# Optimization experiments

Measured on AMD Instinct MI355X. Metric: run time of the kernel, lower is better.

Reference implementation:

```python
import jax, jax.numpy as jnp
import numpy as np

FORWARD_BITS = 8
R_MAX = 0.01
SIGMA0_FWD = 2.0 ** (6 - FORWARD_BITS)  # 0.25, per DynamicFixedQuantizer.__init__


def _rescale(data, sigma, bit, r_max):
    """Dynamic range adjustment: doubles sigma on overflow, halves on underflow."""
    half = 2.0 ** (bit - 1)
    t_max = sigma * half - sigma
    t_min = -sigma * half
    n = jnp.float32(data.size)
    overflow = (jnp.sum(data > t_max) + jnp.sum(data < t_min)).astype(jnp.float32) / n
    underflow = (jnp.sum(data > 0.5 * t_max) + jnp.sum(data < 0.5 * t_min)).astype(jnp.float32) / n
    sigma = jnp.where(overflow > r_max, sigma * 2.0,
                      jnp.where(underflow < r_max, sigma * 0.5, sigma))
    t_max = sigma * half - sigma
    t_min = -sigma * half
    return sigma, t_min, t_max


def _stochastic_round(data, sigma, t_min, t_max, key):
    # temp = floor(data/sigma + U[0,1)) * sigma, then clamp -- fused elementwise chain
    r = jax.random.uniform(key, data.shape, dtype=data.dtype)
    temp = jnp.floor(data / sigma + r) * sigma
    return jnp.clip(temp, t_min, t_max)


def setup_inputs() -> dict:
    key = jax.random.key(0)
    x = jax.random.normal(key, (32, 2048, 2048), dtype=jnp.float32)
    return {"x": x}


def reference(x):
    sigma = jnp.float32(SIGMA0_FWD)
    sigma, t_min, t_max = _rescale(x, sigma, FORWARD_BITS, R_MAX)
    # forward always uses stochastic rounding in the original code
    rkey = jax.random.fold_in(jax.random.key(42), 0)
    return _stochastic_round(x, sigma, t_min, t_max, rkey)
```

## Files before the change

### kernel.cpp

```cpp
#include <hip/hip_runtime.h>
#include <stdint.h>

typedef float floatx4 __attribute__((ext_vector_type(4)));

static inline void threefry2x32_host(uint32_t k0, uint32_t k1,
                                     uint32_t x0, uint32_t x1,
                                     uint32_t& o0, uint32_t& o1) {
  const uint32_t ks2 = k0 ^ k1 ^ 0x1BD11BDAu;
#define TF_ROUND(r) { x0 += x1; x1 = (x1 << (r)) | (x1 >> (32 - (r))); x1 ^= x0; }
  x0 += k0; x1 += k1;
  TF_ROUND(13) TF_ROUND(15) TF_ROUND(26) TF_ROUND(6)
  x0 += k1;  x1 += ks2 + 1u;
  TF_ROUND(17) TF_ROUND(29) TF_ROUND(16) TF_ROUND(24)
  x0 += ks2; x1 += k0 + 2u;
  TF_ROUND(13) TF_ROUND(15) TF_ROUND(26) TF_ROUND(6)
  x0 += k0;  x1 += k1 + 3u;
  TF_ROUND(17) TF_ROUND(29) TF_ROUND(16) TF_ROUND(24)
  x0 += k1;  x1 += ks2 + 4u;
  TF_ROUND(13) TF_ROUND(15) TF_ROUND(26) TF_ROUND(6)
  x0 += ks2; x1 += k0 + 5u;
#undef TF_ROUND
  o0 = x0; o1 = x1;
}

__device__ __forceinline__ uint32_t tf_bits(uint32_t x1, uint32_t k0,
                                            uint32_t k1, uint32_t ks2) {
  uint32_t x0 = k0;
#define R4(a,b,c,d)                                              \
  x0 += x1; x1 = __builtin_rotateleft32(x1, a); x1 ^= x0;        \
  x0 += x1; x1 = __builtin_rotateleft32(x1, b); x1 ^= x0;        \
  x0 += x1; x1 = __builtin_rotateleft32(x1, c); x1 ^= x0;        \
  x0 += x1; x1 = __builtin_rotateleft32(x1, d); x1 ^= x0;
  R4(13, 15, 26, 6)
  x0 += k1;  x1 += ks2 + 1u;
  R4(17, 29, 16, 24)
  x0 += ks2; x1 += k0 + 2u;
  R4(13, 15, 26, 6)
  x0 += k0;  x1 += k1 + 3u;
  R4(17, 29, 16, 24)
  x0 += k1;  x1 += ks2 + 4u;
  R4(13, 15, 26, 6)
  x0 += ks2; x1 += k0 + 5u;
#undef R4
  return x0 ^ x1;
}

__device__ __forceinline__ float qround(float v, uint32_t bits, float sigma,
                                        float inv_sigma, float tmin, float tmax) {
  float r = __uint_as_float((bits >> 9) | 0x3f800000u) - 1.0f;
  float t = floorf(__builtin_fmaf(v, inv_sigma, r)) * sigma;
  return fminf(fmaxf(t, tmin), tmax);
}

__global__ __launch_bounds__(256) void count_kernel(
    const float4* __restrict__ x4, const float* __restrict__ x,
    long long n4, long long n, unsigned int* __restrict__ counts,
    float tmax, float tmin, float htmax, float htmin) {
  long long idx = (long long)blockIdx.x * 256 + threadIdx.x;
  long long stride = (long long)gridDim.x * 256;
  unsigned int over = 0, under = 0;
  for (long long i = idx; i < n4; i += stride) {
    float4 v = x4[i];
    over  += __popcll(__ballot(v.x > tmax))  + __popcll(__ballot(v.x < tmin))
           + __popcll(__ballot(v.y > tmax))  + __popcll(__ballot(v.y < tmin))
           + __popcll(__ballot(v.z > tmax))  + __popcll(__ballot(v.z < tmin))
           + __popcll(__ballot(v.w > tmax))  + __popcll(__ballot(v.w < tmin));
    under += __popcll(__ballot(v.x > htmax)) + __popcll(__ballot(v.x < htmin))
           + __popcll(__ballot(v.y > htmax)) + __popcll(__ballot(v.y < htmin))
           + __popcll(__ballot(v.z > htmax)) + __popcll(__ballot(v.z < htmin))
           + __popcll(__ballot(v.w > htmax)) + __popcll(__ballot(v.w < htmin));
  }
  if ((threadIdx.x & 63) == 0) {
    if (over)  atomicAdd(&counts[0], over);
    if (under) atomicAdd(&counts[1], under);
  }
  if (idx == 0 && (n & 3)) {
    unsigned int o2 = 0, u2 = 0;
    for (long long j = n4 << 2; j < n; ++j) {
      float v = x[j];
      o2 += (v > tmax)  + (v < tmin);
      u2 += (v > htmax) + (v < htmin);
    }
    if (o2) atomicAdd(&counts[0], o2);
    if (u2) atomicAdd(&counts[1], u2);
  }
}

__global__ __launch_bounds__(256) void quant_kernel(
    const float4* __restrict__ x4, floatx4* __restrict__ o4,
    const float* __restrict__ x, float* __restrict__ out,
    long long n4, long long n, const unsigned int* __restrict__ counts,
    float inv_n, uint32_t k0, uint32_t k1) {
  const uint32_t ks2 = k0 ^ k1 ^ 0x1BD11BDAu;
  float overflow  = (float)counts[0] * inv_n;
  float underflow = (float)counts[1] * inv_n;
  float sigma = (overflow > 0.01f) ? 0.5f
              : ((underflow < 0.01f) ? 0.125f : 0.25f);
  float tmax = sigma * 128.0f - sigma;
  float tmin = sigma * -128.0f;
  float inv_sigma = 1.0f / sigma;

  long long idx = (long long)blockIdx.x * 256 + threadIdx.x;
  long long stride = (long long)gridDim.x * 256;
  if (idx < n4) {
    long long i = idx + ((n4 - 1 - idx) / stride) * stride;
    for (; i >= idx; i -= stride) {
      float4 v = x4[i];
      uint32_t s = ((uint32_t)i << 2) + k1;
      uint32_t b0 = tf_bits(s + 0u, k0, k1, ks2);
      uint32_t b1 = tf_bits(s + 1u, k0, k1, ks2);
      uint32_t b2 = tf_bits(s + 2u, k0, k1, ks2);
      uint32_t b3 = tf_bits(s + 3u, k0, k1, ks2);
      floatx4 r;
      r.x = qround(v.x, b0, sigma, inv_sigma, tmin, tmax);
      r.y = qround(v.y, b1, sigma, inv_sigma, tmin, tmax);
      r.z = qround(v.z, b2, sigma, inv_sigma, tmin, tmax);
      r.w = qround(v.w, b3, sigma, inv_sigma, tmin, tmax);
      __builtin_nontemporal_store(r, &o4[i]);
    }
  }
  if (idx == 0 && (n & 3)) {
    for (long long j = n4 << 2; j < n; ++j) {
      uint32_t b = tf_bits((uint32_t)j + k1, k0, k1, ks2);
      out[j] = qround(x[j], b, sigma, inv_sigma, tmin, tmax);
    }
  }
}

extern "C" void kernel_launch(void* const* d_in, const int* in_sizes, int n_in,
                              void* d_out, int out_size, void* d_ws, size_t ws_size,
                              hipStream_t stream) {
  const float* x = (const float*)d_in[0];
  float* out = (float*)d_out;
  long long n = (long long)in_sizes[0];

  unsigned int* counts = (unsigned int*)d_ws;
  (void)hipMemsetAsync(counts, 0, 2 * sizeof(unsigned int), stream);

  uint32_t k0, k1;
  threefry2x32_host(0u, 42u, 0u, 0u, k0, k1);

  const float sigma0 = 0.25f;
  const float tmax0 = sigma0 * 128.0f - sigma0;
  const float tmin0 = -sigma0 * 128.0f;
  const float htmax0 = 0.5f * tmax0;
  const float htmin0 = 0.5f * tmin0;

  long long n4 = n >> 2;
  long long grid = (n4 + 255) / 256;
  if (grid < 1) grid = 1;
  if (grid > 2048) grid = 2048;

  count_kernel<<<(dim3)(unsigned)grid, 256, 0, stream>>>(
      (const float4*)x, x, n4, n, counts, tmax0, tmin0, htmax0, htmin0);

  float inv_n = 1.0f / (float)n;
  quant_kernel<<<(dim3)(unsigned)grid, 256, 0, stream>>>(
      (const float4*)x, (floatx4*)out, x, out, n4, n, counts, inv_n, k0, k1);
}
```

Before: 1.075 ms.

## Fuse count and quantize with speculative sigma, add conditional fixup pass

Merges the counting pass and the quantization pass into one kernel that guesses the final sigma (0.125) and writes the output in the same sweep as the overflow/underflow counts. A single-thread resolve kernel then computes the real sigma, and a fixup kernel redoes the quantization only if the guess was wrong. For inputs where the guess holds, this avoids a second full read of the input. The cost is a full re-quantization when it does not, plus two extra small launches. The fused kernel also uses one element per thread with no grid cap, and the output stores are no longer nontemporal.

Result: faster. 878.3 us (-18.3%).

```diff
diff --git a/kernel.cpp b/kernel.cpp
--- a/kernel.cpp
+++ b/kernel.cpp
@@ -52,72 +52,97 @@
   return fminf(fmaxf(t, tmin), tmax);
 }
 
-__global__ __launch_bounds__(256) void count_kernel(
-    const float4* __restrict__ x4, const float* __restrict__ x,
+__global__ __launch_bounds__(256) void fused_kernel(
+    const float4* __restrict__ x4, floatx4* __restrict__ o4,
+    const float* __restrict__ x, float* __restrict__ out,
     long long n4, long long n, unsigned int* __restrict__ counts,
-    float tmax, float tmin, float htmax, float htmin) {
-  long long idx = (long long)blockIdx.x * 256 + threadIdx.x;
-  long long stride = (long long)gridDim.x * 256;
+    uint32_t k0, uint32_t k1) {
+  const uint32_t ks2 = k0 ^ k1 ^ 0x1BD11BDAu;
+  const float sigma = 0.125f, inv_sigma = 8.0f;
+  const float tmax = 15.875f, tmin = -16.0f;
+  const float ctmax = 31.75f, ctmin = -32.0f;
+  const float chtmax = 15.875f, chtmin = -16.0f;
+
+  long long i = (long long)blockIdx.x * 256 + threadIdx.x;
   unsigned int over = 0, under = 0;
-  for (long long i = idx; i < n4; i += stride) {
+  if (i < n4) {
     float4 v = x4[i];
-    over  += __popcll(__ballot(v.x > tmax))  + __popcll(__ballot(v.x < tmin))
-           + __popcll(__ballot(v.y > tmax))  + __popcll(__ballot(v.y < tmin))
-           + __popcll(__ballot(v.z > tmax))  + __popcll(__ballot(v.z < tmin))
-           + __popcll(__ballot(v.w > tmax))  + __popcll(__ballot(v.w < tmin));
-    under += __popcll(__ballot(v.x > htmax)) + __popcll(__ballot(v.x < htmin))
-           + __popcll(__ballot(v.y > htmax)) + __popcll(__ballot(v.y < htmin))
-           + __popcll(__ballot(v.z > htmax)) + __popcll(__ballot(v.z < htmin))
-           + __popcll(__ballot(v.w > htmax)) + __popcll(__ballot(v.w < htmin));
+    over  = __popcll(__ballot(v.x > ctmax))  + __popcll(__ballot(v.x < ctmin))
+          + __popcll(__ballot(v.y > ctmax))  + __popcll(__ballot(v.y < ctmin))
+          + __popcll(__ballot(v.z > ctmax))  + __popcll(__ballot(v.z < ctmin))
+          + __popcll(__ballot(v.w > ctmax))  + __popcll(__ballot(v.w < ctmin));
+    under = __popcll(__ballot(v.x > chtmax)) + __popcll(__ballot(v.x < chtmin))
+          + __popcll(__ballot(v.y > chtmax)) + __popcll(__ballot(v.y < chtmin))
+          + __popcll(__ballot(v.z > chtmax)) + __popcll(__ballot(v.z < chtmin))
+          + __popcll(__ballot(v.w > chtmax)) + __popcll(__ballot(v.w < chtmin));
+    uint32_t s = ((uint32_t)i << 2) + k1;
+    uint32_t b0 = tf_bits(s + 0u, k0, k1, ks2);
+    uint32_t b1 = tf_bits(s + 1u, k0, k1, ks2);
+    uint32_t b2 = tf_bits(s + 2u, k0, k1, ks2);
+    uint32_t b3 = tf_bits(s + 3u, k0, k1, ks2);
+    floatx4 r;
+    r.x = qround(v.x, b0, sigma, inv_sigma, tmin, tmax);
+    r.y = qround(v.y, b1, sigma, inv_sigma, tmin, tmax);
+    r.z = qround(v.z, b2, sigma, inv_sigma, tmin, tmax);
+    r.w = qround(v.w, b3, sigma, inv_sigma, tmin, tmax);
+    o4[i] = r;
   }
   if ((threadIdx.x & 63) == 0) {
     if (over)  atomicAdd(&counts[0], over);
     if (under) atomicAdd(&counts[1], under);
   }
-  if (idx == 0 && (n & 3)) {
+  if (i == 0 && (n & 3)) {
     unsigned int o2 = 0, u2 = 0;
     for (long long j = n4 << 2; j < n; ++j) {
       float v = x[j];
-      o2 += (v > tmax)  + (v < tmin);
-      u2 += (v > htmax) + (v < htmin);
+      o2 += (v > ctmax)  + (v < ctmin);
+      u2 += (v > chtmax) + (v < chtmin);
+      uint32_t b = tf_bits((uint32_t)j + k1, k0, k1, ks2);
+      out[j] = qround(v, b, sigma, inv_sigma, tmin, tmax);
     }
     if (o2) atomicAdd(&counts[0], o2);
     if (u2) atomicAdd(&counts[1], u2);
   }
 }
 
-__global__ __launch_bounds__(256) void quant_kernel(
-    const float4* __restrict__ x4, floatx4* __restrict__ o4,
-    const float* __restrict__ x, float* __restrict__ out,
-    long long n4, long long n, const unsigned int* __restrict__ counts,
-    float inv_n, uint32_t k0, uint32_t k1) {
-  const uint32_t ks2 = k0 ^ k1 ^ 0x1BD11BDAu;
+__global__ void resolve_kernel(const unsigned int* __restrict__ counts,
+                               unsigned int* __restrict__ flag,
+                               float* __restrict__ params, float inv_n) {
   float overflow  = (float)counts[0] * inv_n;
   float underflow = (float)counts[1] * inv_n;
   float sigma = (overflow > 0.01f) ? 0.5f
               : ((underflow < 0.01f) ? 0.125f : 0.25f);
-  float tmax = sigma * 128.0f - sigma;
-  float tmin = sigma * -128.0f;
-  float inv_sigma = 1.0f / sigma;
+  flag[0] = (sigma != 0.125f) ? 1u : 0u;
+  params[0] = sigma;
+  params[1] = 1.0f / sigma;
+  params[2] = sigma * -128.0f;
+  params[3] = sigma * 128.0f - sigma;
+}
 
+__global__ __launch_bounds__(256) void fixup_kernel(
+    const float4* __restrict__ x4, floatx4* __restrict__ o4,
+    const float* __restrict__ x, float* __restrict__ out,
+    long long n4, long long n, const unsigned int* __restrict__ flag,
+    const float* __restrict__ params, uint32_t k0, uint32_t k1) {
+  if (flag[0] == 0u) return;
+  const uint32_t ks2 = k0 ^ k1 ^ 0x1BD11BDAu;
+  float sigma = params[0], inv_sigma = params[1];
+  float tmin = params[2], tmax = params[3];
   long long idx = (long long)blockIdx.x * 256 + threadIdx.x;
   long long stride = (long long)gridDim.x * 256;
-  if (idx < n4) {
-    long long i = idx + ((n4 - 1 - idx) / stride) * stride;
-    for (; i >= idx; i -= stride) {
-      float4 v = x4[i];
-      uint32_t s = ((uint32_t)i << 2) + k1;
-      uint32_t b0 = tf_bits(s + 0u, k0, k1, ks2);
-      uint32_t b1 = tf_bits(s + 1u, k0, k1, ks2);
-      uint32_t b2 = tf_bits(s + 2u, k0, k1, ks2);
-      uint32_t b3 = tf_bits(s + 3u, k0, k1, ks2);
-      floatx4 r;
-      r.x = qround(v.x, b0, sigma, inv_sigma, tmin, tmax);
-      r.y = qround(v.y, b1, sigma, inv_sigma, tmin, tmax);
-      r.z = qround(v.z, b2, sigma, inv_sigma, tmin, tmax);
-      r.w = qround(v.w, b3, sigma, inv_sigma, tmin, tmax);
-      __builtin_nontemporal_store(r, &o4[i]);
-    }
+  for (long long i = idx; i < n4; i += stride) {
+    float4 v = x4[i];
+    uint32_t s = ((uint32_t)i << 2) + k1;
+    uint32_t b0 = tf_bits(s + 0u, k0, k1, ks2);
+    uint32_t b1 = tf_bits(s + 1u, k0, k1, ks2);
+    uint32_t b2 = tf_bits(s + 2u, k0, k1, ks2);
+    uint32_t b3 = tf_bits(s + 3u, k0, k1, ks2);
+    floatx4 r;
+    r.x = qround(v.x, b0, sigma, inv_sigma, tmin, tmax);
+    r.y = qround(v.y, b1, sigma, inv_sigma, tmin, tmax);
+    r.z = qround(v.z, b2, sigma, inv_sigma, tmin, tmax);
+    r.w = qround(v.w, b3, sigma, inv_sigma, tmin, tmax);
+    o4[i] = r;
   }
   if (idx == 0 && (n & 3)) {
     for (long long j = n4 << 2; j < n; ++j) {
@@ -135,26 +160,25 @@
   long long n = (long long)in_sizes[0];
 
   unsigned int* counts = (unsigned int*)d_ws;
+  unsigned int* flag = counts + 2;
+  float* params = (float*)(counts + 4);
   (void)hipMemsetAsync(counts, 0, 2 * sizeof(unsigned int), stream);
 
   uint32_t k0, k1;
   threefry2x32_host(0u, 42u, 0u, 0u, k0, k1);
 
-  const float sigma0 = 0.25f;
-  const float tmax0 = sigma0 * 128.0f - sigma0;
-  const float tmin0 = -sigma0 * 128.0f;
-  const float htmax0 = 0.5f * tmax0;
-  const float htmin0 = 0.5f * tmin0;
-
   long long n4 = n >> 2;
   long long grid = (n4 + 255) / 256;
   if (grid < 1) grid = 1;
-  if (grid > 2048) grid = 2048;
 
-  count_kernel<<<(dim3)(unsigned)grid, 256, 0, stream>>>(
-      (const float4*)x, x, n4, n, counts, tmax0, tmin0, htmax0, htmin0);
+  fused_kernel<<<(dim3)(unsigned)grid, 256, 0, stream>>>(
+      (const float4*)x, (floatx4*)out, x, out, n4, n, counts, k0, k1);
 
   float inv_n = 1.0f / (float)n;
-  quant_kernel<<<(dim3)(unsigned)grid, 256, 0, stream>>>(
-      (const float4*)x, (floatx4*)out, x, out, n4, n, counts, inv_n, k0, k1);
+  resolve_kernel<<<1, 1, 0, stream>>>(counts, flag, params, inv_n);
+
+  long long gridf = grid;
+  if (gridf > 2048) gridf = 2048;
+  fixup_kernel<<<(dim3)(unsigned)gridf, 256, 0, stream>>>(
+      (const float4*)x, (floatx4*)out, x, out, n4, n, flag, params, k0, k1);
 }
```
